# Performance work log

Hardware: AMD Instinct MI355X
Metric: run time of the kernel (lower is better)

## Reference

```python
import jax, jax.numpy as jnp
import numpy as np

DT_MIN, DT_MAX = 0.001, 0.1
N_STATE = 64


def setup_inputs() -> dict:
    key = jax.random.key(0)
    ks = jax.random.split(key, 8)
    d_model, d_state, Bsz, L = 512, N_STATE, 16, 4096
    A = jax.random.normal(ks[0], (d_state, d_state), jnp.float32) / np.sqrt(d_state)
    A = A - jnp.eye(d_state, dtype=jnp.float32) * 1.5
    return {
        "u": jax.random.normal(ks[1], (Bsz, L, d_model), jnp.float32),
        "A": A,
        "B": jax.random.normal(ks[2], (d_state, 1), jnp.float32) / np.sqrt(d_state),
        "C": jax.random.normal(ks[3], (1, d_state), jnp.float32) / np.sqrt(d_state),
        "D": jax.random.normal(ks[4], (1,), jnp.float32),
        "log_dt": jnp.array([(np.log(DT_MIN) + np.log(DT_MAX)) / 2.0], jnp.float32),
        "W_in": jax.random.normal(ks[5], (1, d_model), jnp.float32) / np.sqrt(d_model),
        "W_out": jax.random.normal(ks[6], (d_model, 1), jnp.float32),
    }


def _s4_forward(u, A, B, C, D, log_dt, W_in, W_out):
    N = A.shape[0]
    dt = jnp.clip(jnp.exp(log_dt[0]), DT_MIN, DT_MAX)
    dA = dt * A                                   # (N, N)
    A_bar = jax.scipy.linalg.expm(dA)             # (N, N)
    B_bar = jnp.linalg.inv(dA) @ (A_bar - jnp.eye(N, dtype=A.dtype)) @ (dt * B)  # (N, 1)

    u_proj = u @ W_in.T                           # (Bsz, L, 1)

    # Original double loop computes x_k = sum_{i<k} A_bar^{k-1-i} B_bar u_i,
    # i.e. x_0 = 0,  x_k = A_bar x_{k-1} + B_bar u_{k-1}  (input enters with one-step delay).
    Bb = B_bar[:, 0]                              # (N,)
    u_seq = jnp.swapaxes(u_proj, 0, 1)            # (L, Bsz, 1)

    def step(x, u_t):
        # emit current state x_k, then advance with u_k
        x_new = x @ A_bar.T + u_t * Bb[None, :]   # (Bsz, N)
        return x_new, x

    x0 = jnp.zeros((u.shape[0], N), u.dtype)
    _, states = jax.lax.scan(step, x0, u_seq)     # (L, Bsz, N)
    states = jnp.swapaxes(states, 0, 1)           # (Bsz, L, N)

    y = states @ C.T + D * u_proj                 # (Bsz, L, 1)
    return y @ W_out.T                            # (Bsz, L, d_model)


def reference(u, A, B, C, D, log_dt, W_in, W_out):
    return _s4_forward(u, A, B, C, D, log_dt, W_in, W_out)
```

## Files before the change

### kernel.cpp

```cpp
#include <hip/hip_runtime.h>
#include <math.h>


#define S0 (Lh)
#define S1 (Lh + 4096)
#define S2 (Lh + 8192)
#define S3 (Lh + 12288)

__device__ __forceinline__ void mm64_core(const float* XT, const float* Y,
                                          int i0, int j0, float c[4][4]) {
#pragma unroll 4
  for (int l = 0; l < 64; ++l) {
    float4 xv = *(const float4*)(XT + l * 64 + i0);
    float4 yv = *(const float4*)(Y + l * 64 + j0);
    c[0][0] += xv.x * yv.x; c[0][1] += xv.x * yv.y; c[0][2] += xv.x * yv.z; c[0][3] += xv.x * yv.w;
    c[1][0] += xv.y * yv.x; c[1][1] += xv.y * yv.y; c[1][2] += xv.y * yv.z; c[1][3] += xv.y * yv.w;
    c[2][0] += xv.z * yv.x; c[2][1] += xv.z * yv.y; c[2][2] += xv.z * yv.z; c[2][3] += xv.z * yv.w;
    c[3][0] += xv.w * yv.x; c[3][1] += xv.w * yv.y; c[3][2] += xv.w * yv.z; c[3][3] += xv.w * yv.w;
  }
}

__device__ __forceinline__ void store_tile(float* Cp, int i0, int j0, float c[4][4]) {
#pragma unroll
  for (int r = 0; r < 4; ++r)
    *(float4*)(Cp + (i0 + r) * 64 + j0) = make_float4(c[r][0], c[r][1], c[r][2], c[r][3]);
}

__device__ __forceinline__ void chain64(const float* rowsrc, float* ubuf,
                                        float* outT, int ln, float v0) {
  float row[64];
#pragma unroll
  for (int q = 0; q < 16; ++q) {
    float4 rv = *(const float4*)(rowsrc + ln * 64 + 4 * q);
    row[4 * q] = rv.x; row[4 * q + 1] = rv.y; row[4 * q + 2] = rv.z; row[4 * q + 3] = rv.w;
  }
  float v = v0;
  for (int jq = 0; jq < 16; ++jq) {
    float q0 = v, q1, q2, q3;
#pragma unroll
    for (int m = 1; m < 4; ++m) {
      ubuf[ln] = v;
      __builtin_amdgcn_wave_barrier();
      float a0 = 0.f, a1 = 0.f, a2 = 0.f, a3 = 0.f;
#pragma unroll
      for (int q = 0; q < 16; ++q) {
        float4 uv = *(const float4*)(ubuf + 4 * q);
        a0 += row[4 * q] * uv.x; a1 += row[4 * q + 1] * uv.y;
        a2 += row[4 * q + 2] * uv.z; a3 += row[4 * q + 3] * uv.w;
      }
      __builtin_amdgcn_wave_barrier();
      v = (a0 + a1) + (a2 + a3);
      if (m == 1) q1 = v; else if (m == 2) q2 = v; else q3 = v;
    }
    *(float4*)(outT + ln * 64 + 4 * jq) = make_float4(q0, q1, q2, q3);
    if (jq < 15) {
      ubuf[ln] = v;
      __builtin_amdgcn_wave_barrier();
      float a0 = 0.f, a1 = 0.f, a2 = 0.f, a3 = 0.f;
#pragma unroll
      for (int q = 0; q < 16; ++q) {
        float4 uv = *(const float4*)(ubuf + 4 * q);
        a0 += row[4 * q] * uv.x; a1 += row[4 * q + 1] * uv.y;
        a2 += row[4 * q + 2] * uv.z; a3 += row[4 * q + 3] * uv.w;
      }
      __builtin_amdgcn_wave_barrier();
      v = (a0 + a1) + (a2 + a3);
    }
  }
}

extern "C" __global__ __launch_bounds__(256) void s4_k1(
    const float* __restrict__ u, const float* __restrict__ A, const float* __restrict__ B,
    const float* __restrict__ C, const float* __restrict__ logdt, const float* __restrict__ Win,
    float* __restrict__ p_ws, float* __restrict__ h_ws) {
  __shared__ __align__(16) float Lh[16384];
  __shared__ __align__(16) float cbuf[64];
  const int tid = threadIdx.x;

  if (blockIdx.x == 0) {
    float dt = expf(logdt[0]);
    dt = fminf(fmaxf(dt, 0.001f), 0.1f);

#pragma unroll
    for (int n = 0; n < 16; ++n) {
      int e = tid * 16 + n;
      int i = e >> 6, j = e & 63;
      float v = A[e] * dt;
      S0[e] = v;
      S1[j * 64 + i] = v;
    }
    __syncthreads();

    const int i0 = (tid & 15) << 2, j0 = (tid >> 4) << 2;
    const int bi = tid & 63, bq = tid >> 6;
    const int wv = tid >> 6, ln = tid & 63;

    float ab[4][4];
#pragma unroll
    for (int r = 0; r < 4; ++r) {
      float4 da = *(const float4*)(S0 + (i0 + r) * 64 + j0);
      ab[r][0] = da.x + ((i0 + r) == (j0 + 0) ? 1.f : 0.f);
      ab[r][1] = da.y + ((i0 + r) == (j0 + 1) ? 1.f : 0.f);
      ab[r][2] = da.z + ((i0 + r) == (j0 + 2) ? 1.f : 0.f);
      ab[r][3] = da.w + ((i0 + r) == (j0 + 3) ? 1.f : 0.f);
    }

    float Bv[16];
#pragma unroll
    for (int m = 0; m < 16; m += 4) {
      float4 b4 = *(const float4*)(B + bq * 16 + m);
      Bv[m] = b4.x; Bv[m + 1] = b4.y; Bv[m + 2] = b4.z; Bv[m + 3] = b4.w;
    }
    float bbp = (bq == (bi >> 4)) ? B[bi] : 0.f;
#pragma unroll
    for (int m = 0; m < 16; m += 4) {
      float4 a4 = *(const float4*)(S0 + bi * 64 + bq * 16 + m);
      bbp += 0.5f * (a4.x * Bv[m] + a4.y * Bv[m + 1] + a4.z * Bv[m + 2] + a4.w * Bv[m + 3]);
    }

    float fact = 1.f;
    int ping = 1;
    for (int k = 2; k <= 5; ++k) {
      const float* Yp = Lh + 4096 * ping;
      float* Cp = Lh + 4096 * (3 - ping);
      float c[4][4] = {{0.f}};
      mm64_core(S0, Yp, i0, j0, c);
      store_tile(Cp, i0, j0, c);
      __syncthreads();
      fact *= (float)k;
      float ivf = 1.f / fact;
      float ivf1 = ivf / (float)(k + 1);
#pragma unroll
      for (int s = 0; s < 4; ++s) {
        float4 pv = *(const float4*)(Cp + (j0 + s) * 64 + i0);
        ab[0][s] += pv.x * ivf; ab[1][s] += pv.y * ivf;
        ab[2][s] += pv.z * ivf; ab[3][s] += pv.w * ivf;
      }
#pragma unroll
      for (int m = 0; m < 16; ++m)
        bbp += ivf1 * Cp[(bq * 16 + m) * 64 + bi] * Bv[m];
      ping = 3 - ping;
    }
    __syncthreads();
    S1[bq * 64 + bi] = bbp;
    __syncthreads();
    float breg = 0.f;
    if (tid < 64)
      breg = dt * (S1[tid] + S1[64 + tid] + S1[128 + tid] + S1[192 + tid]);
    __syncthreads();
    store_tile(S1, i0, j0, ab);
#pragma unroll
    for (int s = 0; s < 4; ++s)
      *(float4*)(S2 + (j0 + s) * 64 + i0) = make_float4(ab[0][s], ab[1][s], ab[2][s], ab[3][s]);
    __syncthreads();

    if (wv == 0) {
      float uq0, uq1, uq2, uq3;
      float uv = C[ln];
      uq0 = uv;
#pragma unroll
      for (int stp = 1; stp < 4; ++stp) {
        cbuf[ln] = uv;
        __builtin_amdgcn_wave_barrier();
        float a0 = 0.f, a1 = 0.f, a2 = 0.f, a3 = 0.f;
#pragma unroll
        for (int q = 0; q < 16; ++q) {
          float4 rv = *(const float4*)(S2 + ln * 64 + 4 * q);
          float4 xv = *(const float4*)(cbuf + 4 * q);
          a0 += rv.x * xv.x; a1 += rv.y * xv.y; a2 += rv.z * xv.z; a3 += rv.w * xv.w;
        }
        __builtin_amdgcn_wave_barrier();
        uv = (a0 + a1) + (a2 + a3);
        if (stp == 1) uq1 = uv; else if (stp == 2) uq2 = uv; else uq3 = uv;
      }
      *(float4*)(S3 + ln * 64) = make_float4(uq0, uq1, uq2, uq3);
    }
    __syncthreads();

    int sM = 1, sT = 2, sF = 0;
    for (int sq = 0; sq < 6; ++sq) {
      {
        float c[4][4] = {{0.f}};
        mm64_core(Lh + 4096 * sT, Lh + 4096 * sM, i0, j0, c);
        store_tile(Lh + 4096 * sF, i0, j0, c);
      }
      __syncthreads();
      if (sq >= 1 && sq <= 4) {
        const int R = 4 << (sq - 1);
        if (i0 < R) {
          float c2[4][4] = {{0.f}};
          mm64_core(S3, Lh + 4096 * sF, i0, j0, c2);
#pragma unroll
          for (int s = 0; s < 4; ++s)
            *(float4*)(S3 + (j0 + s) * 64 + R + i0) =
                make_float4(c2[0][s], c2[1][s], c2[2][s], c2[3][s]);
        }
      }
      if (sq < 5) {
        const float* F = Lh + 4096 * sF;
        float* Dst = Lh + 4096 * sM;
        float4 v0 = *(const float4*)(F + (i0 + 0) * 64 + j0);
        float4 v1 = *(const float4*)(F + (i0 + 1) * 64 + j0);
        float4 v2 = *(const float4*)(F + (i0 + 2) * 64 + j0);
        float4 v3 = *(const float4*)(F + (i0 + 3) * 64 + j0);
        *(float4*)(Dst + (j0 + 0) * 64 + i0) = make_float4(v0.x, v1.x, v2.x, v3.x);
        *(float4*)(Dst + (j0 + 1) * 64 + i0) = make_float4(v0.y, v1.y, v2.y, v3.y);
        *(float4*)(Dst + (j0 + 2) * 64 + i0) = make_float4(v0.z, v1.z, v2.z, v3.z);
        *(float4*)(Dst + (j0 + 3) * 64 + i0) = make_float4(v0.w, v1.w, v2.w, v3.w);
        __syncthreads();
        int nM = sF, nT = sM, nF = sT;
        sM = nM; sT = nT; sF = nF;
      }
    }
    if (wv == 0) chain64(S1, cbuf, S0, ln, breg);
    __syncthreads();

    {
      float c[4][4] = {{0.f}};
      mm64_core(S3, S0, i0, j0, c);
#pragma unroll
      for (int s = 0; s < 4; ++s)
        *(float4*)(h_ws + 64 * (j0 + s) + i0) = make_float4(c[0][s], c[1][s], c[2][s], c[3][s]);
    }
  } else {
    const int pb = blockIdx.x - 1;
    const int ln = tid & 63;
    const int g = (pb << 2) | (tid >> 6);
    float4 w0 = *(const float4*)(Win + ln * 8);
    float4 w1 = *(const float4*)(Win + ln * 8 + 4);
    const size_t base = (size_t)g * 8 * 512 + (size_t)ln * 8;
    float acc[8];
#pragma unroll
    for (int i = 0; i < 8; ++i) {
      const float* up = u + base + (size_t)i * 512;
      float4 a0 = *(const float4*)up;
      float4 a1 = *(const float4*)(up + 4);
      acc[i] = a0.x * w0.x + a0.y * w0.y + a0.z * w0.z + a0.w * w0.w +
               a1.x * w1.x + a1.y * w1.y + a1.z * w1.z + a1.w * w1.w;
    }
#pragma unroll
    for (int off = 32; off > 0; off >>= 1) {
#pragma unroll
      for (int i = 0; i < 8; ++i) acc[i] += __shfl_xor(acc[i], off);
    }
    if (ln == 0) {
      *(float4*)(p_ws + (g << 3)) = make_float4(acc[0], acc[1], acc[2], acc[3]);
      *(float4*)(p_ws + (g << 3) + 4) = make_float4(acc[4], acc[5], acc[6], acc[7]);
    }
  }
}

extern "C" __global__ __launch_bounds__(512) void s4_conv(
    const float* __restrict__ p_ws, const float* __restrict__ h_ws,
    const float* __restrict__ Dp, float* __restrict__ sv_ws) {
  __shared__ __align__(16) float hpad[4352];
  __shared__ __align__(16) float ps[4096];
  __shared__ __align__(16) float part[2048];
  const int tid = threadIdx.x;
  const int b = blockIdx.x >> 4, tile = blockIdx.x & 15;

  if (tid < 256) hpad[tid] = 0.f;
#pragma unroll
  for (int i = 0; i < 2; ++i) {
    int idx = i * 2048 + tid * 4;
    *(float4*)(hpad + 256 + idx) = *(const float4*)(h_ws + idx);
    *(float4*)(ps + idx) = *(const float4*)(p_ws + (b << 12) + idx);
  }
  __syncthreads();

  const int wv = tid >> 6, ln = tid & 63;
  const int t0 = tile << 8;
  float a0 = 0.f, a1 = 0.f, a2 = 0.f, a3 = 0.f;
  for (int c = wv; c <= tile; c += 8) {
    const float* pA = hpad + 256 + t0 + 4 * ln - 4 - (c << 8);
    const float* pc = ps + (c << 8);
#pragma unroll 4
    for (int k = 0; k < 256; k += 4) {
      float4 p4 = *(const float4*)(pc + k);
      float4 hA = *(const float4*)(pA - k);
      float4 hB = *(const float4*)(pA - k + 4);
      a0 += p4.x * hA.w + p4.y * hA.z + p4.z * hA.y + p4.w * hA.x;
      a1 += p4.x * hB.x + p4.y * hA.w + p4.z * hA.z + p4.w * hA.y;
      a2 += p4.x * hB.y + p4.y * hB.x + p4.z * hA.w + p4.w * hA.z;
      a3 += p4.x * hB.z + p4.y * hB.y + p4.z * hB.x + p4.w * hA.w;
    }
  }
  *(float4*)(part + (wv << 8) + (ln << 2)) = make_float4(a0, a1, a2, a3);
  __syncthreads();
  if (tid < 256) {
    float s = Dp[0] * ps[t0 + tid];
#pragma unroll
    for (int w = 0; w < 8; ++w) s += part[w * 256 + tid];
    sv_ws[(b << 12) + t0 + tid] = s;
  }
}

extern "C" __global__ __launch_bounds__(256) void s4_out(
    const float* __restrict__ sv_ws, const float* __restrict__ Wout,
    float* __restrict__ out) {
  const int tid = threadIdx.x;
  const int ln = tid & 63;
  const int g = (blockIdx.x << 2) | (tid >> 6);
  float4 wa = *(const float4*)(Wout + ln * 8);
  float4 wb = *(const float4*)(Wout + ln * 8 + 4);
  float myv = sv_ws[(g << 3) + (ln & 7)];
  float* op0 = out + (size_t)(g << 3) * 512 + (size_t)ln * 8;
#pragma unroll
  for (int i = 0; i < 8; ++i) {
    float s = __shfl(myv, i);
    float* op = op0 + (size_t)i * 512;
    *(float4*)op = make_float4(s * wa.x, s * wa.y, s * wa.z, s * wa.w);
    *(float4*)(op + 4) = make_float4(s * wb.x, s * wb.y, s * wb.z, s * wb.w);
  }
}

extern "C" void kernel_launch(void* const* d_in, const int* in_sizes, int n_in,
                              void* d_out, int out_size, void* d_ws, size_t ws_size,
                              hipStream_t stream) {
  const float* u = (const float*)d_in[0];
  const float* A = (const float*)d_in[1];
  const float* B = (const float*)d_in[2];
  const float* C = (const float*)d_in[3];
  const float* D = (const float*)d_in[4];
  const float* logdt = (const float*)d_in[5];
  const float* Win = (const float*)d_in[6];
  const float* Wout = (const float*)d_in[7];
  float* outp = (float*)d_out;
  float* p_ws = (float*)d_ws;
  float* h_ws = p_ws + 65536;
  float* sv_ws = h_ws + 4096;

  s4_k1<<<2049, 256, 0, stream>>>(u, A, B, C, logdt, Win, p_ws, h_ws);
  s4_conv<<<256, 512, 0, stream>>>(p_ws, h_ws, D, sv_ws);
  s4_out<<<2048, 256, 0, stream>>>(sv_ws, Wout, outp);
}
```

Baseline: 293.5 us.

## Fuse causal convolution with output projection and retile conv into finer blocks

Merges the convolution and output-broadcast kernels into one kernel, removing the intermediate scalar buffer and one launch. Each block now covers 32 timesteps instead of 256, giving 2048 blocks, and splits the inner reduction across 8 k-groups per wave so the causal triangle is load-balanced. The cost is that every block reloads the full 4096-entry impulse response and the batch input sequence into shared memory (about 32KB per block), which is repeated across many more blocks, and the blocks also do a larger partial-sum reduction.

```diff
diff --git a/kernel.cpp b/kernel.cpp
--- a/kernel.cpp
+++ b/kernel.cpp
@@ -250,32 +250,34 @@
   }
 }
 
-extern "C" __global__ __launch_bounds__(512) void s4_conv(
+extern "C" __global__ __launch_bounds__(512) void s4_co(
     const float* __restrict__ p_ws, const float* __restrict__ h_ws,
-    const float* __restrict__ Dp, float* __restrict__ sv_ws) {
-  __shared__ __align__(16) float hpad[4352];
+    const float* __restrict__ Dp, const float* __restrict__ Wout,
+    float* __restrict__ out) {
+  __shared__ __align__(16) float hpad[4608];
   __shared__ __align__(16) float ps[4096];
   __shared__ __align__(16) float part[2048];
+  __shared__ __align__(16) float svs[32];
   const int tid = threadIdx.x;
-  const int b = blockIdx.x >> 4, tile = blockIdx.x & 15;
-
-  if (tid < 256) hpad[tid] = 0.f;
-#pragma unroll
-  for (int i = 0; i < 2; ++i) {
-    int idx = i * 2048 + tid * 4;
-    *(float4*)(hpad + 256 + idx) = *(const float4*)(h_ws + idx);
-    *(float4*)(ps + idx) = *(const float4*)(p_ws + (b << 12) + idx);
-  }
+  const int b = blockIdx.x >> 7, tile = blockIdx.x & 127;
+  const int t0 = tile << 5;
+
+  if (tid < 128) *(float4*)(hpad + tid * 4) = make_float4(0.f, 0.f, 0.f, 0.f);
+  *(float4*)(hpad + 512 + tid * 8) = *(const float4*)(h_ws + tid * 8);
+  *(float4*)(hpad + 512 + tid * 8 + 4) = *(const float4*)(h_ws + tid * 8 + 4);
+  *(float4*)(ps + tid * 8) = *(const float4*)(p_ws + (b << 12) + tid * 8);
+  *(float4*)(ps + tid * 8 + 4) = *(const float4*)(p_ws + (b << 12) + tid * 8 + 4);
   __syncthreads();
 
   const int wv = tid >> 6, ln = tid & 63;
-  const int t0 = tile << 8;
+  const int og = ln & 7, kg = ln >> 3;
+  const int cmax = (t0 + 31) >> 8;
   float a0 = 0.f, a1 = 0.f, a2 = 0.f, a3 = 0.f;
-  for (int c = wv; c <= tile; c += 8) {
-    const float* pA = hpad + 256 + t0 + 4 * ln - 4 - (c << 8);
-    const float* pc = ps + (c << 8);
-#pragma unroll 4
-    for (int k = 0; k < 256; k += 4) {
+  for (int c = wv; c <= cmax; c += 8) {
+    const float* pA = hpad + 512 + t0 + 4 * og - 4 - (c << 8) - (kg << 5);
+    const float* pc = ps + (c << 8) + (kg << 5);
+#pragma unroll
+    for (int k = 0; k < 32; k += 4) {
       float4 p4 = *(const float4*)(pc + k);
       float4 hA = *(const float4*)(pA - k);
       float4 hB = *(const float4*)(pA - k + 4);
@@ -285,30 +287,28 @@
       a3 += p4.x * hB.z + p4.y * hB.y + p4.z * hB.x + p4.w * hA.w;
     }
   }
-  *(float4*)(part + (wv << 8) + (ln << 2)) = make_float4(a0, a1, a2, a3);
+  *(float4*)(part + (tid << 2)) = make_float4(a0, a1, a2, a3);
   __syncthreads();
-  if (tid < 256) {
+  if (tid < 32) {
     float s = Dp[0] * ps[t0 + tid];
-#pragma unroll
-    for (int w = 0; w < 8; ++w) s += part[w * 256 + tid];
-    sv_ws[(b << 12) + t0 + tid] = s;
-  }
-}
-
-extern "C" __global__ __launch_bounds__(256) void s4_out(
-    const float* __restrict__ sv_ws, const float* __restrict__ Wout,
-    float* __restrict__ out) {
-  const int tid = threadIdx.x;
-  const int ln = tid & 63;
-  const int g = (blockIdx.x << 2) | (tid >> 6);
+    const int o4 = tid >> 2, oc = tid & 3;
+#pragma unroll
+    for (int wvi = 0; wvi < 8; ++wvi)
+#pragma unroll
+      for (int kgi = 0; kgi < 8; ++kgi)
+        s += part[(((wvi << 6) + (kgi << 3) + o4) << 2) + oc];
+    svs[tid] = s;
+  }
+  __syncthreads();
+
   float4 wa = *(const float4*)(Wout + ln * 8);
   float4 wb = *(const float4*)(Wout + ln * 8 + 4);
-  float myv = sv_ws[(g << 3) + (ln & 7)];
-  float* op0 = out + (size_t)(g << 3) * 512 + (size_t)ln * 8;
-#pragma unroll
-  for (int i = 0; i < 8; ++i) {
-    float s = __shfl(myv, i);
-    float* op = op0 + (size_t)i * 512;
+  const size_t rowbase = ((size_t)(b << 12) + (size_t)t0) * 512 + (size_t)ln * 8;
+#pragma unroll
+  for (int r4 = 0; r4 < 4; ++r4) {
+    const int r = (wv << 2) + r4;
+    float s = svs[r];
+    float* op = out + rowbase + (size_t)r * 512;
     *(float4*)op = make_float4(s * wa.x, s * wa.y, s * wa.z, s * wa.w);
     *(float4*)(op + 4) = make_float4(s * wb.x, s * wb.y, s * wb.z, s * wb.w);
   }
@@ -328,9 +328,7 @@
   float* outp = (float*)d_out;
   float* p_ws = (float*)d_ws;
   float* h_ws = p_ws + 65536;
-  float* sv_ws = h_ws + 4096;
 
   s4_k1<<<2049, 256, 0, stream>>>(u, A, B, C, logdt, Win, p_ws, h_ws);
-  s4_conv<<<256, 512, 0, stream>>>(p_ws, h_ws, D, sv_ws);
-  s4_out<<<2048, 256, 0, stream>>>(sv_ws, Wout, outp);
-}
+  s4_co<<<2048, 512, 0, stream>>>(p_ws, h_ws, D, Wout, outp);
+}
```

Result: faster. 273.6 us (-6.8%).
